# Kernel tuning notes

Measured on AMD Instinct MI355X. Metric: run time of the kernel, lower is better.

## Reference

```python
import jax, jax.numpy as jnp
import numpy as np
from jax import lax

TEMP = 0.1
EPS_LOG = 1e-6
RMS_EPS = 1e-6
K_NEIGHBORS = 8


def setup_inputs() -> dict:
    key = jax.random.key(0)
    ks = jax.random.split(key, 8)
    B, T, D = 2, 2048, 1024
    N, DK, DM = 32768, 256, 256
    return {
        "x": jax.random.normal(ks[0], (B, T, D), dtype=jnp.float32),
        "keys": jax.random.normal(ks[1], (N, DK), dtype=jnp.float32),
        "vals": jax.random.normal(ks[2], (N, DM), dtype=jnp.float32),
        "W_in": jax.random.normal(ks[3], (DK, D), dtype=jnp.float32) / np.sqrt(D),
        "b_in": jnp.zeros((DK,), dtype=jnp.float32),
        "W_out": jax.random.normal(ks[4], (D, K_NEIGHBORS * DM), dtype=jnp.float32) / np.sqrt(K_NEIGHBORS * DM),
        "b_out": jnp.zeros((D,), dtype=jnp.float32),
        "rms_w": jnp.ones((D,), dtype=jnp.float32),
    }


def _memory_forward(x, keys, vals, W_in, b_in, W_out, b_out, rms_w):
    B, T, D = x.shape
    N, DM = vals.shape
    # proj_in: [B,T,D] -> [B,T,DK]
    q = jnp.einsum("btd,kd->btk", x, W_in) + b_in
    # squared euclidean distances to memory keys: [B,T,N]
    q2 = jnp.sum(q * q, axis=-1, keepdims=True)          # [B,T,1]
    k2 = jnp.sum(keys * keys, axis=-1)                   # [N]
    qk = jnp.einsum("btc,nc->btn", q, keys)              # [B,T,N]
    logits = -(q2 - 2.0 * qk + k2) / TEMP                # [B,T,N]

    # N3Net-style continuous k-NN: k rounds of softmax selection
    def step(lg, _):
        w = jax.nn.softmax(lg, axis=-1)                  # [B,T,N]
        out = jnp.einsum("btn,nf->btf", w, vals)         # [B,T,DM]
        lg = lg + jnp.log1p(-w + EPS_LOG)
        return lg, out

    _, outs = lax.scan(step, logits, None, length=K_NEIGHBORS)  # [K,B,T,DM]
    nearest = jnp.moveaxis(outs, 0, 2).reshape(B, T, K_NEIGHBORS * DM)

    out = jnp.einsum("btf,df->btd", nearest, W_out) + b_out
    # RMSNorm
    var = jnp.mean(out.astype(jnp.float32) ** 2, axis=-1, keepdims=True)
    out = out * lax.rsqrt(var + RMS_EPS)
    return rms_w * out


def reference(x, keys, vals, W_in, b_in, W_out, b_out, rms_w):
    return _memory_forward(x, keys, vals, W_in, b_in, W_out, b_out, rms_w)
```

## Files before the change

kernel.cpp:

```cpp
#include <hip/hip_runtime.h>
#include <hip/hip_bf16.h>

#define ROWS  4096
#define DDIM  1024
#define DKDIM 256
#define NKEYS 32768
#define DMDIM 256
#define KN    8
#define FDIM  2048
#define CAPS  1536
#define SURV  128
#define MARGIN 16.0f

typedef float  f32x4  __attribute__((ext_vector_type(4)));
typedef __bf16 bf16x8 __attribute__((ext_vector_type(8)));

static __device__ __forceinline__ unsigned enc_f32(float f) {
  unsigned u = __float_as_uint(f);
  return u ^ ((unsigned)((int)u >> 31) | 0x80000000u);
}
static __device__ __forceinline__ float dec_f32(unsigned u) {
  unsigned b = (u & 0x80000000u) ? (u ^ 0x80000000u) : ~u;
  return __uint_as_float(b);
}
static __device__ __forceinline__ unsigned short f2bf(float f) {
  unsigned u = __float_as_uint(f);
  u += 0x7FFFu + ((u >> 16) & 1u);
  return (unsigned short)(u >> 16);
}
static __device__ __forceinline__ unsigned pack_cand(float s, int n) {
  float q = (s + 1024.f) * 64.f;
  int u = (int)q;
  u = u < 0 ? 0 : (u > 131071 ? 131071 : u);
  return ((unsigned)u << 15) | (unsigned)n;
}
static __device__ __forceinline__ float cand_score(unsigned p) {
  return (float)(p >> 15) * (1.f / 64.f) - 1024.f;
}
static __device__ __forceinline__ void gld16(const void* g, void* l) {
  __builtin_amdgcn_global_load_lds((const __attribute__((address_space(1))) void*)g,
                                   (__attribute__((address_space(3))) void*)l, 16, 0, 0);
}

__global__ __launch_bounds__(256) void prep_keys(const float* __restrict__ keys,
                                                 unsigned short* __restrict__ kbf,
                                                 float* __restrict__ k2) {
  const int row = blockIdx.x * 4 + (threadIdx.x >> 6);
  const int ln  = threadIdx.x & 63;
  const float4 v = *(const float4*)(keys + (size_t)row * DKDIM + ln * 4);
  ushort4 o;
  o.x = f2bf(v.x); o.y = f2bf(v.y); o.z = f2bf(v.z); o.w = f2bf(v.w);
  *(ushort4*)(kbf + (size_t)row * DKDIM + ln * 4) = o;
  float ss = v.x*v.x + v.y*v.y + v.z*v.z + v.w*v.w;
  for (int off = 32; off; off >>= 1) ss += __shfl_down(ss, off);
  if (ln == 0) k2[row] = ss;
}

__global__ __launch_bounds__(256) void cvt_bf16(const float* __restrict__ src,
                                                unsigned short* __restrict__ dst, int n4) {
  const int i = blockIdx.x * 256 + threadIdx.x;
  if (i < n4) {
    const float4 v = *(const float4*)(src + (size_t)i * 4);
    ushort4 o;
    o.x = f2bf(v.x); o.y = f2bf(v.y); o.z = f2bf(v.z); o.w = f2bf(v.w);
    *(ushort4*)(dst + (size_t)i * 4) = o;
  }
}

__global__ __launch_bounds__(256) void qproj(const float* __restrict__ x,
                                             const float* __restrict__ Win,
                                             const float* __restrict__ bin,
                                             float* __restrict__ qf,
                                             unsigned short* __restrict__ qbf) {
  __shared__ __align__(16) float As[64][68];
  __shared__ __align__(16) float Bs[64][68];
  const int bm = blockIdx.x, bn = blockIdx.y;
  const int t  = threadIdx.x;
  const int tx = t & 15, ty = t >> 4;
  float acc[4][4] = {};
  for (int ks = 0; ks < 16; ++ks) {
    __syncthreads();
    for (int l = t; l < 1024; l += 256) {
      const int row = l >> 4, kc = l & 15;
      *(float4*)(&As[row][kc * 4]) =
          *(const float4*)(x + (size_t)(bm * 64 + row) * DDIM + ks * 64 + kc * 4);
      *(float4*)(&Bs[row][kc * 4]) =
          *(const float4*)(Win + (size_t)(bn * 64 + row) * DDIM + ks * 64 + kc * 4);
    }
    __syncthreads();
    for (int kk = 0; kk < 64; kk += 4) {
      float4 av[4], bv[4];
#pragma unroll
      for (int i = 0; i < 4; ++i) av[i] = *(const float4*)(&As[ty * 4 + i][kk]);
#pragma unroll
      for (int j = 0; j < 4; ++j) bv[j] = *(const float4*)(&Bs[tx * 4 + j][kk]);
#pragma unroll
      for (int i = 0; i < 4; ++i)
#pragma unroll
        for (int j = 0; j < 4; ++j)
          acc[i][j] += av[i].x * bv[j].x + av[i].y * bv[j].y +
                       av[i].z * bv[j].z + av[i].w * bv[j].w;
    }
  }
#pragma unroll
  for (int i = 0; i < 4; ++i)
#pragma unroll
    for (int j = 0; j < 4; ++j) {
      const int m = bm * 64 + ty * 4 + i, n = bn * 64 + tx * 4 + j;
      const float q = acc[i][j] + bin[n];
      qf[(size_t)m * DKDIM + n] = q;
      qbf[(size_t)m * DKDIM + n] = f2bf(q);
    }
}

template <int KD>
static __device__ __forceinline__ void gemm_tile(const unsigned short* __restrict__ A,
                                                 const unsigned short* __restrict__ B,
                                                 int bm, int bn,
                                                 unsigned short* As, unsigned short* Bs,
                                                 f32x4 acc[4][4]) {
  const int tid  = threadIdx.x;
  const int lane = tid & 63, wave = tid >> 6;
  const int quad = lane >> 4, l15 = lane & 15;
  const int wr = (wave >> 1) * 64, wc = (wave & 1) * 64;
  const int srow = tid >> 2, skc = tid & 3;
  const unsigned short* gA = A + (size_t)(bm * 128 + srow) * KD + skc * 8;
  const unsigned short* gB = B + (size_t)(bn * 128 + srow) * KD + skc * 8;
  for (int ks = 0; ks < KD / 32; ++ks) {
    __syncthreads();
    gld16(gA + ks * 32,                     As + tid * 8);
    gld16(gA + (size_t)64 * KD + ks * 32,   As + 2048 + tid * 8);
    gld16(gB + ks * 32,                     Bs + tid * 8);
    gld16(gB + (size_t)64 * KD + ks * 32,   Bs + 2048 + tid * 8);
    __syncthreads();
    bf16x8 af[4], bfr[4];
#pragma unroll
    for (int i = 0; i < 4; ++i)
      af[i] = *(const bf16x8*)(As + (wr + i * 16 + l15) * 32 + quad * 8);
#pragma unroll
    for (int j = 0; j < 4; ++j)
      bfr[j] = *(const bf16x8*)(Bs + (wc + j * 16 + l15) * 32 + quad * 8);
#pragma unroll
    for (int i = 0; i < 4; ++i)
#pragma unroll
      for (int j = 0; j < 4; ++j)
        acc[i][j] = __builtin_amdgcn_mfma_f32_16x16x32_bf16(af[i], bfr[j], acc[i][j], 0, 0, 0);
  }
}

__global__ __launch_bounds__(256) void score_select(const unsigned short* __restrict__ qbf,
                                                    const unsigned short* __restrict__ kbf,
                                                    const float* __restrict__ k2,
                                                    unsigned* __restrict__ rowmax,
                                                    int* __restrict__ cnt,
                                                    unsigned* __restrict__ cand) {
  __shared__ __align__(16) unsigned short As[4096];
  __shared__ __align__(16) unsigned short Bs[4096];
  __shared__ float wm[128][2];
  __shared__ float thr[128];
  f32x4 acc[4][4] = {};
  gemm_tile<DKDIM>(qbf, kbf, blockIdx.x, blockIdx.y, As, Bs, acc);
  const int t = threadIdx.x;
  const int lane = t & 63, wave = t >> 6;
  const int quad = lane >> 4, l15 = lane & 15;
  const int wr = (wave >> 1) * 64, wc = (wave & 1) * 64;
  float k2v[4];
#pragma unroll
  for (int j = 0; j < 4; ++j) k2v[j] = k2[blockIdx.y * 128 + wc + j * 16 + l15];
#pragma unroll
  for (int i = 0; i < 4; ++i)
#pragma unroll
    for (int r = 0; r < 4; ++r) {
      float v = -3.4e38f;
#pragma unroll
      for (int j = 0; j < 4; ++j) v = fmaxf(v, 2.f * acc[i][j][r] - k2v[j]);
      for (int m = 8; m; m >>= 1) v = fmaxf(v, __shfl_xor(v, m));
      if (l15 == 0) wm[wr + i * 16 + quad * 4 + r][wave & 1] = v;
    }
  __syncthreads();
  if (t < 128) {
    const float tile = fmaxf(wm[t][0], wm[t][1]);
    const unsigned old = atomicMax(&rowmax[blockIdx.x * 128 + t], enc_f32(tile));
    thr[t] = fmaxf(tile, dec_f32(old)) - MARGIN;
  }
  __syncthreads();
#pragma unroll
  for (int i = 0; i < 4; ++i)
#pragma unroll
    for (int r = 0; r < 4; ++r) {
      const int rl = wr + i * 16 + quad * 4 + r;
      const float th = thr[rl];
      const int gm = blockIdx.x * 128 + rl;
#pragma unroll
      for (int j = 0; j < 4; ++j) {
        const float s = 2.f * acc[i][j][r] - k2v[j];
        if (s >= th) {
          const int n = blockIdx.y * 128 + wc + j * 16 + l15;
          const int pos = atomicAdd(&cnt[gm], 1);
          if (pos < CAPS) cand[(size_t)gm * CAPS + pos] = pack_cand(s, n);
        }
      }
    }
}

__global__ __launch_bounds__(256) void knn_rounds(const float* __restrict__ qf,
                                                  const float* __restrict__ keys,
                                                  const float* __restrict__ k2,
                                                  const float* __restrict__ vals,
                                                  const int* __restrict__ cnt,
                                                  const unsigned* __restrict__ cand,
                                                  unsigned short* __restrict__ nearest) {
  __shared__ __align__(16) float qs[DKDIM];
  __shared__ unsigned cl[CAPS];
  __shared__ float red[256];
  __shared__ int   sidx[SURV];
  __shared__ float Ls[SURV];
  __shared__ float cs[SURV];
  __shared__ float Ws[SURV * KN];
  __shared__ int nsurv;
  const int row = blockIdx.x, t = threadIdx.x;
  const int C = min(cnt[row], CAPS);
  qs[t] = qf[(size_t)row * DKDIM + t];
  if (t == 0) nsurv = 0;
  float m = -3.4e38f;
  for (int i = t; i < C; i += 256) {
    const unsigned p = cand[(size_t)row * CAPS + i];
    cl[i] = p;
    m = fmaxf(m, cand_score(p));
  }
  red[t] = m;
  __syncthreads();
  for (int s = 128; s; s >>= 1) {
    if (t < s) red[t] = fmaxf(red[t], red[t + s]);
    __syncthreads();
  }
  const float th = red[0] - 14.0f;
  for (int i = t; i < C; i += 256) {
    if (cand_score(cl[i]) >= th) {
      const int p = atomicAdd(&nsurv, 1);
      if (p < SURV) sidx[p] = (int)(cl[i] & 32767u);
    }
  }
  if (t < SURV) cs[t] = 0.f;
  __syncthreads();
  const int S = min(nsurv, SURV);
  const int wv = t >> 6, ln = t & 63;
  for (int i = wv; i < S; i += 4) {
    const int n = sidx[i];
    const float4 kv = *(const float4*)(keys + (size_t)n * DKDIM + ln * 4);
    const float4 qv = *(const float4*)(qs + ln * 4);
    float d = kv.x * qv.x + kv.y * qv.y + kv.z * qv.z + kv.w * qv.w;
    for (int o = 32; o; o >>= 1) d += __shfl_down(d, o);
    if (ln == 0) Ls[i] = (2.f * d - k2[n]) / 0.1f;
  }
  __syncthreads();
  if (t < 64) {
    for (int j = 0; j < KN; ++j) {
      float lm = -3.4e38f;
      for (int i = t; i < S; i += 64) lm = fmaxf(lm, Ls[i] + cs[i]);
      for (int o = 32; o; o >>= 1) lm = fmaxf(lm, __shfl_xor(lm, o));
      float zs = 0.f;
      for (int i = t; i < S; i += 64) {
        const float e = expf(Ls[i] + cs[i] - lm);
        Ws[i * KN + j] = e; zs += e;
      }
      for (int o = 32; o; o >>= 1) zs += __shfl_xor(zs, o);
      const float Zi = 1.f / zs;
      for (int i = t; i < S; i += 64) {
        const float w = Ws[i * KN + j] * Zi;
        Ws[i * KN + j] = w;
        cs[i] += log1pf(1e-6f - w);
      }
    }
  }
  __syncthreads();
  float acc[KN] = {};
  for (int i = 0; i < S; ++i) {
    const float v = vals[(size_t)sidx[i] * DMDIM + t];
#pragma unroll
    for (int j = 0; j < KN; ++j) acc[j] += Ws[i * KN + j] * v;
  }
#pragma unroll
  for (int j = 0; j < KN; ++j)
    nearest[(size_t)row * FDIM + j * DMDIM + t] = f2bf(acc[j]);
}

__global__ __launch_bounds__(256) void out_gemm(const unsigned short* __restrict__ nbf,
                                                const unsigned short* __restrict__ wbf,
                                                const float* __restrict__ bout,
                                                float* __restrict__ out) {
  __shared__ __align__(16) unsigned short As[4096];
  __shared__ __align__(16) unsigned short Bs[4096];
  f32x4 acc[4][4] = {};
  gemm_tile<FDIM>(nbf, wbf, blockIdx.x, blockIdx.y, As, Bs, acc);
  const int lane = threadIdx.x & 63, wave = threadIdx.x >> 6;
  const int quad = lane >> 4, l15 = lane & 15;
  const int wr = (wave >> 1) * 64, wc = (wave & 1) * 64;
#pragma unroll
  for (int i = 0; i < 4; ++i)
#pragma unroll
    for (int r = 0; r < 4; ++r) {
      const int gm = blockIdx.x * 128 + wr + i * 16 + quad * 4 + r;
#pragma unroll
      for (int j = 0; j < 4; ++j) {
        const int n = blockIdx.y * 128 + wc + j * 16 + l15;
        out[(size_t)gm * DDIM + n] = acc[i][j][r] + bout[n];
      }
    }
}

__global__ __launch_bounds__(256) void rmsnorm(float* __restrict__ out,
                                               const float* __restrict__ rmsw) {
  __shared__ float red[256];
  const int row = blockIdx.x, t = threadIdx.x;
  const float4 v = *(const float4*)(out + (size_t)row * DDIM + t * 4);
  red[t] = v.x * v.x + v.y * v.y + v.z * v.z + v.w * v.w;
  __syncthreads();
  for (int s = 128; s; s >>= 1) {
    if (t < s) red[t] += red[t + s];
    __syncthreads();
  }
  const float scale = rsqrtf(red[0] / (float)DDIM + 1e-6f);
  const float4 w = *(const float4*)(rmsw + t * 4);
  float4 o;
  o.x = v.x * scale * w.x; o.y = v.y * scale * w.y;
  o.z = v.z * scale * w.z; o.w = v.w * scale * w.w;
  *(float4*)(out + (size_t)row * DDIM + t * 4) = o;
}

extern "C" void kernel_launch(void* const* d_in, const int* in_sizes, int n_in,
                              void* d_out, int out_size, void* d_ws, size_t ws_size,
                              hipStream_t stream) {
  const float* x    = (const float*)d_in[0];
  const float* keys = (const float*)d_in[1];
  const float* vals = (const float*)d_in[2];
  const float* Win  = (const float*)d_in[3];
  const float* bin  = (const float*)d_in[4];
  const float* Wout = (const float*)d_in[5];
  const float* bout = (const float*)d_in[6];
  const float* rmsw = (const float*)d_in[7];
  float* out = (float*)d_out;
  char* ws = (char*)d_ws;

  float*          q_f32   = (float*)(ws);
  unsigned short* q_bf    = (unsigned short*)(ws + 4194304);
  unsigned short* k_bf    = (unsigned short*)(ws + 6291456);
  unsigned short* nearest = (unsigned short*)(ws + 6291456);
  float*          k2      = (float*)(ws + 23068672);
  unsigned*       rowmax  = (unsigned*)(ws + 23199744);
  int*            cnt     = (int*)(ws + 23216128);
  unsigned*       cand    = (unsigned*)(ws + 23232512);
  unsigned short* w_bf    = (unsigned short*)(ws + 48398336);

  hipMemsetAsync(rowmax, 0, 32768, stream);

  prep_keys<<<NKEYS / 4, 256, 0, stream>>>(keys, k_bf, k2);
  cvt_bf16<<<(DDIM * FDIM / 4) / 256, 256, 0, stream>>>(Wout, w_bf, DDIM * FDIM / 4);
  qproj<<<dim3(ROWS / 64, DKDIM / 64), 256, 0, stream>>>(x, Win, bin, q_f32, q_bf);
  score_select<<<dim3(ROWS / 128, NKEYS / 128), 256, 0, stream>>>(q_bf, k_bf, k2, rowmax, cnt, cand);
  knn_rounds<<<ROWS, 256, 0, stream>>>(q_f32, keys, k2, vals, cnt, cand, nearest);
  out_gemm<<<dim3(ROWS / 128, DDIM / 128), 256, 0, stream>>>(nearest, w_bf, bout, out);
  rmsnorm<<<ROWS, 256, 0, stream>>>(out, rmsw);
}
```

Baseline: 441.8 us.

## Split score selection into seed-max pass and strip-scanning candidate kernel

Adds a seed_max kernel that computes the row maxima over the first 2048 keys and writes them through atomicMax. A new score_strip kernel then keeps a 64-row query tile resident in LDS, streams 4096 keys per block, and filters candidates against a threshold fixed by the seed max minus a margin. The aim is to cut the over-collection and atomic traffic caused by the weak running-max thresholds of the old per-tile scheme, and to reuse the query tile across many key tiles. The cost is an extra partial GEMM pass plus a serial key loop per block with fewer blocks.

```diff
diff --git a/kernel.cpp b/kernel.cpp
--- a/kernel.cpp
+++ b/kernel.cpp
@@ -148,20 +148,15 @@
   }
 }
 
-__global__ __launch_bounds__(256) void score_select(const unsigned short* __restrict__ qbf,
-                                                    const unsigned short* __restrict__ kbf,
-                                                    const float* __restrict__ k2,
-                                                    unsigned* __restrict__ rowmax,
-                                                    int* __restrict__ cnt,
-                                                    unsigned* __restrict__ cand) {
+__global__ __launch_bounds__(256) void seed_max(const unsigned short* __restrict__ qbf,
+                                                const unsigned short* __restrict__ kbf,
+                                                const float* __restrict__ k2,
+                                                unsigned* __restrict__ rowmax) {
   __shared__ __align__(16) unsigned short As[4096];
   __shared__ __align__(16) unsigned short Bs[4096];
-  __shared__ float wm[128][2];
-  __shared__ float thr[128];
   f32x4 acc[4][4] = {};
   gemm_tile<DKDIM>(qbf, kbf, blockIdx.x, blockIdx.y, As, Bs, acc);
-  const int t = threadIdx.x;
-  const int lane = t & 63, wave = t >> 6;
+  const int lane = threadIdx.x & 63, wave = threadIdx.x >> 6;
   const int quad = lane >> 4, l15 = lane & 15;
   const int wr = (wave >> 1) * 64, wc = (wave & 1) * 64;
   float k2v[4];
@@ -175,32 +170,85 @@
 #pragma unroll
       for (int j = 0; j < 4; ++j) v = fmaxf(v, 2.f * acc[i][j][r] - k2v[j]);
       for (int m = 8; m; m >>= 1) v = fmaxf(v, __shfl_xor(v, m));
-      if (l15 == 0) wm[wr + i * 16 + quad * 4 + r][wave & 1] = v;
-    }
-  __syncthreads();
-  if (t < 128) {
-    const float tile = fmaxf(wm[t][0], wm[t][1]);
-    const unsigned old = atomicMax(&rowmax[blockIdx.x * 128 + t], enc_f32(tile));
-    thr[t] = fmaxf(tile, dec_f32(old)) - MARGIN;
-  }
-  __syncthreads();
-#pragma unroll
-  for (int i = 0; i < 4; ++i)
-#pragma unroll
-    for (int r = 0; r < 4; ++r) {
-      const int rl = wr + i * 16 + quad * 4 + r;
-      const float th = thr[rl];
-      const int gm = blockIdx.x * 128 + rl;
-#pragma unroll
-      for (int j = 0; j < 4; ++j) {
-        const float s = 2.f * acc[i][j][r] - k2v[j];
-        if (s >= th) {
-          const int n = blockIdx.y * 128 + wc + j * 16 + l15;
-          const int pos = atomicAdd(&cnt[gm], 1);
-          if (pos < CAPS) cand[(size_t)gm * CAPS + pos] = pack_cand(s, n);
+      if (l15 == 0) {
+        const int gm = blockIdx.x * 128 + wr + i * 16 + quad * 4 + r;
+        atomicMax(&rowmax[gm], enc_f32(v));
+      }
+    }
+}
+
+__global__ __launch_bounds__(256) void score_strip(const unsigned short* __restrict__ qbf,
+                                                   const unsigned short* __restrict__ kbf,
+                                                   const float* __restrict__ k2,
+                                                   const unsigned* __restrict__ rowmax,
+                                                   int* __restrict__ cnt,
+                                                   unsigned* __restrict__ cand) {
+  __shared__ __align__(16) unsigned short As[64 * 264];
+  __shared__ __align__(16) unsigned short Bs[2 * 4096];
+  __shared__ float thr_s[64];
+  const int t = threadIdx.x;
+  const int bm = blockIdx.x;
+  const int key0 = blockIdx.y * 4096;
+#pragma unroll
+  for (int ii = 0; ii < 8; ++ii) {
+    const int chunk = ii * 256 + t;
+    const int row = chunk >> 5, cir = chunk & 31;
+    *(float4*)(As + row * 264 + cir * 8) =
+        *(const float4*)(qbf + (size_t)(bm * 64 + row) * DKDIM + cir * 8);
+  }
+  if (t < 64) thr_s[t] = dec_f32(rowmax[bm * 64 + t]) - MARGIN;
+  const int lane = t & 63, wave = t >> 6;
+  const int quad = lane >> 4, l15 = lane & 15;
+  const int kh = t >> 2, kc = t & 3;
+  for (int kt = 0; kt < 32; ++kt) {
+    f32x4 acc[4][2] = {};
+    float k2v[2];
+#pragma unroll
+    for (int j = 0; j < 2; ++j)
+      k2v[j] = k2[key0 + kt * 128 + wave * 32 + j * 16 + l15];
+    for (int it = 0; it < 4; ++it) {
+      __syncthreads();
+#pragma unroll
+      for (int s2 = 0; s2 < 2; ++s2)
+#pragma unroll
+        for (int h = 0; h < 2; ++h)
+          gld16(kbf + (size_t)(key0 + kt * 128 + h * 64 + kh) * DKDIM + it * 64 + s2 * 32 + kc * 8,
+                Bs + s2 * 4096 + h * 2048 + t * 8);
+      __syncthreads();
+#pragma unroll
+      for (int s2 = 0; s2 < 2; ++s2) {
+        bf16x8 af[4], bfr[2];
+#pragma unroll
+        for (int i = 0; i < 4; ++i)
+          af[i] = *(const bf16x8*)(As + (i * 16 + l15) * 264 + it * 64 + s2 * 32 + quad * 8);
+#pragma unroll
+        for (int j = 0; j < 2; ++j)
+          bfr[j] = *(const bf16x8*)(Bs + s2 * 4096 + (wave * 32 + j * 16 + l15) * 32 + quad * 8);
+#pragma unroll
+        for (int i = 0; i < 4; ++i)
+#pragma unroll
+          for (int j = 0; j < 2; ++j)
+            acc[i][j] = __builtin_amdgcn_mfma_f32_16x16x32_bf16(af[i], bfr[j], acc[i][j], 0, 0, 0);
+      }
+    }
+#pragma unroll
+    for (int i = 0; i < 4; ++i)
+#pragma unroll
+      for (int r = 0; r < 4; ++r) {
+        const int rl = i * 16 + quad * 4 + r;
+        const float th = thr_s[rl];
+        const int gm = bm * 64 + rl;
+#pragma unroll
+        for (int j = 0; j < 2; ++j) {
+          const float s = 2.f * acc[i][j][r] - k2v[j];
+          if (s >= th) {
+            const int n = key0 + kt * 128 + wave * 32 + j * 16 + l15;
+            const int pos = atomicAdd(&cnt[gm], 1);
+            if (pos < CAPS) cand[(size_t)gm * CAPS + pos] = pack_cand(s, n);
+          }
         }
       }
-    }
+  }
 }
 
 __global__ __launch_bounds__(256) void knn_rounds(const float* __restrict__ qf,
@@ -357,7 +405,8 @@
   prep_keys<<<NKEYS / 4, 256, 0, stream>>>(keys, k_bf, k2);
   cvt_bf16<<<(DDIM * FDIM / 4) / 256, 256, 0, stream>>>(Wout, w_bf, DDIM * FDIM / 4);
   qproj<<<dim3(ROWS / 64, DKDIM / 64), 256, 0, stream>>>(x, Win, bin, q_f32, q_bf);
-  score_select<<<dim3(ROWS / 128, NKEYS / 128), 256, 0, stream>>>(q_bf, k_bf, k2, rowmax, cnt, cand);
+  seed_max<<<dim3(ROWS / 128, 16), 256, 0, stream>>>(q_bf, k_bf, k2, rowmax);
+  score_strip<<<dim3(ROWS / 64, NKEYS / 4096), 256, 0, stream>>>(q_bf, k_bf, k2, rowmax, cnt, cand);
   knn_rounds<<<ROWS, 256, 0, stream>>>(q_f32, keys, k2, vals, cnt, cand, nearest);
   out_gemm<<<dim3(ROWS / 128, DDIM / 128), 256, 0, stream>>>(nearest, w_bf, bout, out);
   rmsnorm<<<ROWS, 256, 0, stream>>>(out, rmsw);
```

After: 509.9 us. +15.4%, slower.

## Merge prep kernels and memset, add exact-logit second filter in kNN rounds

Applied to the files above, without the earlier changes.

Merges key conversion, W_out bf16 conversion and the rowmax zeroing into a single launch, removing two launches and a memset. In knn_rounds, the first-stage bf16 score threshold is tightened and a second filter runs on exact fp32 logits, keeping at most 96 survivors within a fixed margin of the maximum. This reduces the softmax rounds and the vals gather/accumulate work, at the risk of dropping candidates whose weights are not negligible.

```diff
diff --git a/kernel.cpp b/kernel.cpp
--- a/kernel.cpp
+++ b/kernel.cpp
@@ -10,7 +10,10 @@
 #define FDIM  2048
 #define CAPS  1536
 #define SURV  128
-#define MARGIN 16.0f
+#define SURV2 96
+#define MARGIN   16.0f
+#define REFILT_M 12.25f
+#define EXACT_M  109.0f
 
 typedef float  f32x4  __attribute__((ext_vector_type(4)));
 typedef __bf16 bf16x8 __attribute__((ext_vector_type(8)));
@@ -42,28 +45,31 @@
                                    (__attribute__((address_space(3))) void*)l, 16, 0, 0);
 }
 
-__global__ __launch_bounds__(256) void prep_keys(const float* __restrict__ keys,
-                                                 unsigned short* __restrict__ kbf,
-                                                 float* __restrict__ k2) {
-  const int row = blockIdx.x * 4 + (threadIdx.x >> 6);
-  const int ln  = threadIdx.x & 63;
-  const float4 v = *(const float4*)(keys + (size_t)row * DKDIM + ln * 4);
-  ushort4 o;
-  o.x = f2bf(v.x); o.y = f2bf(v.y); o.z = f2bf(v.z); o.w = f2bf(v.w);
-  *(ushort4*)(kbf + (size_t)row * DKDIM + ln * 4) = o;
-  float ss = v.x*v.x + v.y*v.y + v.z*v.z + v.w*v.w;
-  for (int off = 32; off; off >>= 1) ss += __shfl_down(ss, off);
-  if (ln == 0) k2[row] = ss;
-}
-
-__global__ __launch_bounds__(256) void cvt_bf16(const float* __restrict__ src,
-                                                unsigned short* __restrict__ dst, int n4) {
-  const int i = blockIdx.x * 256 + threadIdx.x;
-  if (i < n4) {
-    const float4 v = *(const float4*)(src + (size_t)i * 4);
+__global__ __launch_bounds__(256) void prep_all(const float* __restrict__ keys,
+                                                const float* __restrict__ Wout,
+                                                unsigned short* __restrict__ kbf,
+                                                float* __restrict__ k2,
+                                                unsigned short* __restrict__ wbf,
+                                                unsigned* __restrict__ rowmax) {
+  const int b = blockIdx.x, t = threadIdx.x;
+  if (b < 8192) {
+    const int row = b * 4 + (t >> 6);
+    const int ln  = t & 63;
+    const float4 v = *(const float4*)(keys + (size_t)row * DKDIM + ln * 4);
     ushort4 o;
     o.x = f2bf(v.x); o.y = f2bf(v.y); o.z = f2bf(v.z); o.w = f2bf(v.w);
-    *(ushort4*)(dst + (size_t)i * 4) = o;
+    *(ushort4*)(kbf + (size_t)row * DKDIM + ln * 4) = o;
+    float ss = v.x*v.x + v.y*v.y + v.z*v.z + v.w*v.w;
+    for (int off = 32; off; off >>= 1) ss += __shfl_down(ss, off);
+    if (ln == 0) k2[row] = ss;
+  } else if (b < 10240) {
+    const int i = (b - 8192) * 256 + t;
+    const float4 v = *(const float4*)(Wout + (size_t)i * 4);
+    ushort4 o;
+    o.x = f2bf(v.x); o.y = f2bf(v.y); o.z = f2bf(v.z); o.w = f2bf(v.w);
+    *(ushort4*)(wbf + (size_t)i * 4) = o;
+  } else {
+    rowmax[(b - 10240) * 256 + t] = 0u;
   }
 }
 
@@ -215,13 +221,15 @@
   __shared__ float red[256];
   __shared__ int   sidx[SURV];
   __shared__ float Ls[SURV];
-  __shared__ float cs[SURV];
-  __shared__ float Ws[SURV * KN];
-  __shared__ int nsurv;
+  __shared__ int   sidx2[SURV2];
+  __shared__ float L2v[SURV2];
+  __shared__ float cs[SURV2];
+  __shared__ float Ws[SURV2 * KN];
+  __shared__ int n1, n2;
   const int row = blockIdx.x, t = threadIdx.x;
   const int C = min(cnt[row], CAPS);
   qs[t] = qf[(size_t)row * DKDIM + t];
-  if (t == 0) nsurv = 0;
+  if (t == 0) { n1 = 0; n2 = 0; }
   float m = -3.4e38f;
   for (int i = t; i < C; i += 256) {
     const unsigned p = cand[(size_t)row * CAPS + i];
@@ -234,18 +242,18 @@
     if (t < s) red[t] = fmaxf(red[t], red[t + s]);
     __syncthreads();
   }
-  const float th = red[0] - 14.0f;
+  const float th1 = red[0] - REFILT_M;
   for (int i = t; i < C; i += 256) {
-    if (cand_score(cl[i]) >= th) {
-      const int p = atomicAdd(&nsurv, 1);
+    if (cand_score(cl[i]) >= th1) {
+      const int p = atomicAdd(&n1, 1);
       if (p < SURV) sidx[p] = (int)(cl[i] & 32767u);
     }
   }
-  if (t < SURV) cs[t] = 0.f;
-  __syncthreads();
-  const int S = min(nsurv, SURV);
+  if (t < SURV2) cs[t] = 0.f;
+  __syncthreads();
+  const int S1 = min(n1, SURV);
   const int wv = t >> 6, ln = t & 63;
-  for (int i = wv; i < S; i += 4) {
+  for (int i = wv; i < S1; i += 4) {
     const int n = sidx[i];
     const float4 kv = *(const float4*)(keys + (size_t)n * DKDIM + ln * 4);
     const float4 qv = *(const float4*)(qs + ln * 4);
@@ -254,19 +262,32 @@
     if (ln == 0) Ls[i] = (2.f * d - k2[n]) / 0.1f;
   }
   __syncthreads();
+  red[t] = (t < S1) ? Ls[t] : -3.4e38f;
+  __syncthreads();
+  for (int s = 128; s; s >>= 1) {
+    if (t < s) red[t] = fmaxf(red[t], red[t + s]);
+    __syncthreads();
+  }
+  const float Lmax = red[0];
+  if (t < S1 && Ls[t] >= Lmax - EXACT_M) {
+    const int p = atomicAdd(&n2, 1);
+    if (p < SURV2) { sidx2[p] = sidx[t]; L2v[p] = Ls[t]; }
+  }
+  __syncthreads();
+  const int S2 = min(n2, SURV2);
   if (t < 64) {
     for (int j = 0; j < KN; ++j) {
       float lm = -3.4e38f;
-      for (int i = t; i < S; i += 64) lm = fmaxf(lm, Ls[i] + cs[i]);
+      for (int i = t; i < S2; i += 64) lm = fmaxf(lm, L2v[i] + cs[i]);
       for (int o = 32; o; o >>= 1) lm = fmaxf(lm, __shfl_xor(lm, o));
       float zs = 0.f;
-      for (int i = t; i < S; i += 64) {
-        const float e = expf(Ls[i] + cs[i] - lm);
+      for (int i = t; i < S2; i += 64) {
+        const float e = expf(L2v[i] + cs[i] - lm);
         Ws[i * KN + j] = e; zs += e;
       }
       for (int o = 32; o; o >>= 1) zs += __shfl_xor(zs, o);
       const float Zi = 1.f / zs;
-      for (int i = t; i < S; i += 64) {
+      for (int i = t; i < S2; i += 64) {
         const float w = Ws[i * KN + j] * Zi;
         Ws[i * KN + j] = w;
         cs[i] += log1pf(1e-6f - w);
@@ -275,8 +296,8 @@
   }
   __syncthreads();
   float acc[KN] = {};
-  for (int i = 0; i < S; ++i) {
-    const float v = vals[(size_t)sidx[i] * DMDIM + t];
+  for (int i = 0; i < S2; ++i) {
+    const float v = vals[(size_t)sidx2[i] * DMDIM + t];
 #pragma unroll
     for (int j = 0; j < KN; ++j) acc[j] += Ws[i * KN + j] * v;
   }
@@ -352,10 +373,7 @@
   unsigned*       cand    = (unsigned*)(ws + 23232512);
   unsigned short* w_bf    = (unsigned short*)(ws + 48398336);
 
-  hipMemsetAsync(rowmax, 0, 32768, stream);
-
-  prep_keys<<<NKEYS / 4, 256, 0, stream>>>(keys, k_bf, k2);
-  cvt_bf16<<<(DDIM * FDIM / 4) / 256, 256, 0, stream>>>(Wout, w_bf, DDIM * FDIM / 4);
+  prep_all<<<10272, 256, 0, stream>>>(keys, Wout, k_bf, k2, w_bf, rowmax);
   qproj<<<dim3(ROWS / 64, DKDIM / 64), 256, 0, stream>>>(x, Win, bin, q_f32, q_bf);
   score_select<<<dim3(ROWS / 128, NKEYS / 128), 256, 0, stream>>>(q_bf, k_bf, k2, rowmax, cnt, cand);
   knn_rounds<<<ROWS, 256, 0, stream>>>(q_f32, keys, k2, vals, cnt, cand, nearest);
```

Result: no change. 438.5 us (-0.7%).
